# Performance work log

Measured on AMD Instinct MI355X. Metric: run time of the kernel, lower is better.

The kernel has to match this reference:

```python
import jax, jax.numpy as jnp
import numpy as np

PI = 3.14159  # constant used in the torch module
N_QUBITS = 10
N_LAYERS = 4
B = 1024  # number of graphs


def _lin_init(k, fan_in, fan_out):
    k1, k2 = jax.random.split(k)
    s = 1.0 / np.sqrt(fan_in)
    W = jax.random.uniform(k1, (fan_in, fan_out), jnp.float32, -s, s)
    b = jax.random.uniform(k2, (fan_out,), jnp.float32, -s, s)
    return W, b


def setup_inputs():
    key = jax.random.key(0)
    ks = jax.random.split(key, 12)
    N, E, Fin, H, Emb = 32768, 131072, 128, 256, 128
    x = jax.random.normal(ks[0], (N, Fin), jnp.float32)
    edge_index = jax.random.randint(ks[1], (2, E), 0, N)
    batch = jnp.sort(jax.random.randint(ks[2], (N,), 0, B))
    edge_attr = jax.random.uniform(ks[3], (E, 4), dtype=jnp.float32)
    W1, b1 = _lin_init(ks[4], Fin, H)          # GCNConv 1
    W2, b2 = _lin_init(ks[5], H, Emb)          # GCNConv 2
    projW, projb = _lin_init(ks[6], Emb, N_QUBITS)
    vqc_weights = jax.random.uniform(ks[7], (N_LAYERS, N_QUBITS), jnp.float32, 0.0, 2 * np.pi)
    epW, epb = _lin_init(ks[8], 4, N_QUBITS - 1)
    cW1, cb1 = _lin_init(ks[9], Emb + N_QUBITS, 16)
    cW2, cb2 = _lin_init(ks[10], 16, 1)
    return dict(x=x, edge_index=edge_index, batch=batch, edge_attr=edge_attr,
                W1=W1, b1=b1, W2=W2, b2=b2, projW=projW, projb=projb,
                vqc_weights=vqc_weights, epW=epW, epb=epb,
                cW1=cW1, cb1=cb1, cW2=cW2, cb2=cb2)


def _gcn_conv(x, W, b, src, dst, n):
    # GCNConv with self-loops: sym-normalized aggregation of xW
    h = x @ W
    deg = jnp.zeros((n,), x.dtype).at[dst].add(1.0) + 1.0  # +1 self-loop
    dinv = jax.lax.rsqrt(deg)
    coef = (dinv[src] * dinv[dst])[:, None]
    agg = jnp.zeros_like(h).at[dst].add(h[src] * coef)
    return agg + h * (1.0 / deg)[:, None] + b


def _segment_mean(v, seg, n):
    tot = jnp.zeros((n, v.shape[1]), v.dtype).at[seg].add(v)
    cnt = jnp.zeros((n,), v.dtype).at[seg].add(1.0)
    return tot / jnp.clip(cnt, 1.0)[:, None]


def _run_vqc(q_in, weights, ep):
    # Batched real state-vector simulation. All gates (RY, CRY) are real.
    # Wire 0 = most significant bit (pennylane default.qubit convention).
    b = q_in.shape[0]
    dim = 2 ** N_QUBITS
    st = jnp.zeros((b, dim), q_in.dtype).at[:, 0].set(1.0)

    def ry(st, theta, w):
        th = jnp.broadcast_to(theta, (b,)) * 0.5
        c = jnp.cos(th)[:, None, None]
        s = jnp.sin(th)[:, None, None]
        r = st.reshape(b, 2 ** w, 2, -1)
        a0, a1 = r[:, :, 0], r[:, :, 1]
        return jnp.stack([c * a0 - s * a1, s * a0 + c * a1], axis=2).reshape(b, dim)

    def cry(st, theta, w):
        # control w, target w+1 (adjacent wires)
        th = jnp.broadcast_to(theta, (b,)) * 0.5
        c = jnp.cos(th)[:, None, None]
        s = jnp.sin(th)[:, None, None]
        r = st.reshape(b, 2 ** w, 2, 2, -1)
        a0, a1 = r[:, :, 1, 0], r[:, :, 1, 1]
        r = r.at[:, :, 1, 0].set(c * a0 - s * a1).at[:, :, 1, 1].set(s * a0 + c * a1)
        return r.reshape(b, dim)

    for i in range(N_QUBITS):                      # AngleEmbedding (RY)
        st = ry(st, q_in[:, i], i)
    for layer in range(N_LAYERS):
        for i in range(N_QUBITS):
            st = ry(st, weights[layer, i], i)
        for i in range(N_QUBITS - 1):
            st = cry(st, ep[:, i], i)

    probs = st * st
    zs = []
    for i in range(N_QUBITS):
        p = probs.reshape(b, 2 ** i, 2, -1).sum(axis=(1, 3))
        zs.append(p[:, 0] - p[:, 1])               # <PauliZ(i)>
    return jnp.stack(zs, axis=1)                   # [B, n_qubits]


def reference(x, edge_index, batch, edge_attr, W1, b1, W2, b2, projW, projb,
              vqc_weights, epW, epb, cW1, cb1, cW2, cb2):
    N = x.shape[0]
    src, dst = edge_index[0], edge_index[1]
    # GCN encoder: two GCNConv + ReLU, global mean pool (dropout = eval mode)
    h = jax.nn.relu(_gcn_conv(x, W1, b1, src, dst, N))
    h = jax.nn.relu(_gcn_conv(h, W2, b2, src, dst, N))
    emb = _segment_mean(h, batch, B)               # [B, gcn_embed]

    q_in = jnp.tanh(emb @ projW + projb) * PI      # [B, n_qubits]

    # scatter-mean edge pooling per graph, then edge projection
    edge_batch = batch[src]
    pooled_edge = _segment_mean(edge_attr, edge_batch, B)  # [B, 4]
    ep = pooled_edge @ epW + epb                   # [B, n_qubits-1]

    q_out = _run_vqc(q_in, vqc_weights, ep)        # [B, n_qubits]

    combined = jnp.concatenate([emb, q_out], axis=-1)
    hid = jax.nn.relu(combined @ cW1 + cb1)
    return hid @ cW2 + cb2                         # [B, num_tasks]
```

## Files before the change

### kernel.cpp

```cpp
#include <hip/hip_runtime.h>

#define PI_F 3.14159f
#define NQ 10
#define PB 64

__global__ void k_zero(float4* __restrict__ p, int n4) {
  int i = blockIdx.x * blockDim.x + threadIdx.x;
  int stride = gridDim.x * blockDim.x;
  float4 z = {0.f, 0.f, 0.f, 0.f};
  for (; i < n4; i += stride) p[i] = z;
}

__global__ void k_count(const int* __restrict__ dstA, int E, int* __restrict__ cnt) {
  int e = blockIdx.x * blockDim.x + threadIdx.x;
  if (e < E) atomicAdd(&cnt[dstA[e]], 1);
}

__global__ __launch_bounds__(1024) void k_edge_pool(const int* __restrict__ srcA,
                                                    const int* __restrict__ batch,
                                                    const float* __restrict__ eattr, int E,
                                                    float* __restrict__ part) {
  __shared__ float bins[1024 * 5];
  int t = threadIdx.x;
  for (int i = t; i < 5120; i += 1024) bins[i] = 0.f;
  __syncthreads();
  int per = (E + gridDim.x - 1) / gridDim.x;
  int base = blockIdx.x * per;
  int end = min(base + per, E);
  for (int e = base + t; e < end; e += 1024) {
    int s = srcA[e];
    int g = batch[s];
    float4 v = *(const float4*)(eattr + (size_t)e * 4);
    atomicAdd(&bins[g * 5 + 0], v.x);
    atomicAdd(&bins[g * 5 + 1], v.y);
    atomicAdd(&bins[g * 5 + 2], v.z);
    atomicAdd(&bins[g * 5 + 3], v.w);
    atomicAdd(&bins[g * 5 + 4], 1.0f);
  }
  __syncthreads();
  float* dst = part + (size_t)blockIdx.x * 5120;
  for (int i = t; i < 5120; i += 1024) dst[i] = bins[i];
}

__global__ __launch_bounds__(1024) void k_scan1(const int* __restrict__ cnt,
                                                int* __restrict__ incl,
                                                int* __restrict__ bsum) {
  __shared__ int buf[1024];
  int t = threadIdx.x;
  int base = blockIdx.x << 10;
  buf[t] = cnt[base + t];
  __syncthreads();
#pragma unroll
  for (int off = 1; off < 1024; off <<= 1) {
    int x = (t >= off) ? buf[t - off] : 0;
    __syncthreads();
    buf[t] += x;
    __syncthreads();
  }
  incl[base + t] = buf[t];
  if (t == 1023) bsum[blockIdx.x] = buf[t];
}

__global__ void k_node_setup(const int* __restrict__ cnt, const int* __restrict__ incl,
                             const int* __restrict__ bsum, const int* __restrict__ batch,
                             int N, int Bn, int* __restrict__ rowStart,
                             int* __restrict__ pos, float* __restrict__ dinv,
                             float* __restrict__ invdeg, int* __restrict__ starts) {
  int i = blockIdx.x * blockDim.x + threadIdx.x;
  if (i >= N) return;
  int blk = i >> 10;
  int pre = 0;
  for (int j = 0; j < blk; j++) pre += bsum[j];
  int c = cnt[i];
  int inc = incl[i] + pre;
  rowStart[i + 1] = inc;
  pos[i] = inc - c;
  if (i == 0) rowStart[0] = 0;
  float d = (float)c + 1.0f;
  dinv[i] = 1.0f / sqrtf(d);
  invdeg[i] = 1.0f / d;
  int b = batch[i];
  int bp = (i == 0) ? -1 : batch[i - 1];
  for (int g = bp + 1; g <= b; g++) starts[g] = i;
  if (i == N - 1) {
    for (int g = b + 1; g <= Bn; g++) starts[g] = N;
  }
}

__global__ void k_fill(const int* __restrict__ dst, const int* __restrict__ srcA,
                       const float* __restrict__ dinv, int E, int* __restrict__ pos,
                       int* __restrict__ srcSorted, float* __restrict__ dcoef) {
  int e = blockIdx.x * blockDim.x + threadIdx.x;
  if (e >= E) return;
  int s = srcA[e];
  int slot = atomicAdd(&pos[dst[e]], 1);
  srcSorted[slot] = s;
  dcoef[slot] = dinv[s];
}

__global__ __launch_bounds__(256) void k_gemm(const float* __restrict__ A,
                                              const float* __restrict__ B,
                                              float* __restrict__ C,
                                              int M, int K, int N) {
  __shared__ float As[128][33];
  __shared__ float Bs[32][68];
  int t = threadIdx.x;
  int tx = t & 15, ty = t >> 4;
  int row0 = blockIdx.y * 128, col0 = blockIdx.x * 64;
  float acc[8][4] = {};
  for (int k0 = 0; k0 < K; k0 += 32) {
    __syncthreads();
#pragma unroll
    for (int rep = 0; rep < 4; rep++) {
      int slot = t + rep * 256;
      int r = slot >> 3;
      int cg = (slot & 7) << 2;
      float4 v = *(const float4*)(A + (size_t)(row0 + r) * K + (k0 + cg));
      As[r][cg + 0] = v.x;
      As[r][cg + 1] = v.y;
      As[r][cg + 2] = v.z;
      As[r][cg + 3] = v.w;
    }
#pragma unroll
    for (int rep = 0; rep < 2; rep++) {
      int slot = t + rep * 256;
      int r2 = slot >> 4;
      int c2 = (slot & 15) << 2;
      float4 w = *(const float4*)(B + (size_t)(k0 + r2) * N + (col0 + c2));
      *(float4*)&Bs[r2][c2] = w;
    }
    __syncthreads();
#pragma unroll 4
    for (int kk = 0; kk < 32; kk++) {
      float4 b4 = *(const float4*)&Bs[kk][tx << 2];
      float bv[4] = {b4.x, b4.y, b4.z, b4.w};
      float av[8];
#pragma unroll
      for (int i = 0; i < 8; i++) av[i] = As[(ty << 3) + i][kk];
#pragma unroll
      for (int i = 0; i < 8; i++)
#pragma unroll
        for (int j = 0; j < 4; j++) acc[i][j] = fmaf(av[i], bv[j], acc[i][j]);
    }
  }
#pragma unroll
  for (int i = 0; i < 8; i++) {
    float4 v = {acc[i][0], acc[i][1], acc[i][2], acc[i][3]};
    *(float4*)(C + (size_t)(row0 + (ty << 3) + i) * N + (col0 + (tx << 2))) = v;
  }
}

__global__ __launch_bounds__(256) void k_gcn_combine(
    const float* __restrict__ hlin, const int* __restrict__ srcSorted,
    const float* __restrict__ dcoef, const int* __restrict__ rowStart,
    const float* __restrict__ dinv, const float* __restrict__ invdeg,
    const float* __restrict__ bias, float* __restrict__ hout, int N, int C, int shift) {
  int gid = blockIdx.x * blockDim.x + threadIdx.x;
  int n = gid >> shift;
  if (n >= N) return;
  int cq = (gid & ((1 << shift) - 1)) << 2;
  int e0 = rowStart[n], e1 = rowStart[n + 1];
  float di = dinv[n];
  float ax = 0.f, ay = 0.f, az = 0.f, aw = 0.f;
  for (int e = e0; e < e1; e++) {
    int s = srcSorted[e];
    float coef = dcoef[e] * di;
    float4 v = *(const float4*)(hlin + (size_t)s * C + cq);
    ax = fmaf(coef, v.x, ax);
    ay = fmaf(coef, v.y, ay);
    az = fmaf(coef, v.z, az);
    aw = fmaf(coef, v.w, aw);
  }
  float idg = invdeg[n];
  float4 hv = *(const float4*)(hlin + (size_t)n * C + cq);
  float4 bv = *(const float4*)(bias + cq);
  float4 r;
  r.x = fmaxf(fmaf(hv.x, idg, ax) + bv.x, 0.f);
  r.y = fmaxf(fmaf(hv.y, idg, ay) + bv.y, 0.f);
  r.z = fmaxf(fmaf(hv.z, idg, az) + bv.z, 0.f);
  r.w = fmaxf(fmaf(hv.w, idg, aw) + bv.w, 0.f);
  *(float4*)(hout + (size_t)n * C + cq) = r;
}

__global__ __launch_bounds__(256) void k_segmean(const float* __restrict__ h2,
                                                 const int* __restrict__ starts,
                                                 float* __restrict__ emb) {
  __shared__ float tmp[128];
  int g = blockIdx.x;
  int t = threadIdx.x;
  int c = t & 127;
  int half = t >> 7;
  int s0 = starts[g], s1 = starts[g + 1];
  float inv = 1.0f / (float)(s1 - s0 > 0 ? s1 - s0 : 1);
  float sum = 0.f;
  for (int i = s0 + half; i < s1; i += 2) sum += h2[(size_t)i * 128 + c];
  if (half == 0) tmp[c] = sum;
  __syncthreads();
  if (half == 1) emb[(size_t)g * 128 + c] = (tmp[c] + sum) * inv;
}

__global__ __launch_bounds__(256) void k_angles(
    const float* __restrict__ emb, const float* __restrict__ part,
    const float* __restrict__ projW, const float* __restrict__ projb,
    const float* __restrict__ epW, const float* __restrict__ epb, int Bn,
    float* __restrict__ angc, float* __restrict__ angs) {
  int wid = (blockIdx.x * blockDim.x + threadIdx.x) >> 6;
  int lane = threadIdx.x & 63;
  int g = wid / 11;
  int a = wid - g * 11;
  if (g >= Bn) return;
  if (a < 10) {
    float2 v = *(const float2*)(emb + (size_t)g * 128 + lane * 2);
    float s = v.x * projW[(lane * 2) * NQ + a] + v.y * projW[(lane * 2 + 1) * NQ + a];
#pragma unroll
    for (int off = 32; off >= 1; off >>= 1) s += __shfl_down(s, off, 64);
    if (lane == 0) {
      float th = tanhf(s + projb[a]) * PI_F * 0.5f;
      angc[g * 19 + a] = cosf(th);
      angs[g * 19 + a] = sinf(th);
    }
  } else {
    const float* pp = part + (size_t)lane * 5120 + g * 5;
    float p0 = pp[0], p1 = pp[1], p2 = pp[2], p3 = pp[3], p4 = pp[4];
#pragma unroll
    for (int off = 32; off >= 1; off >>= 1) {
      p0 += __shfl_down(p0, off, 64);
      p1 += __shfl_down(p1, off, 64);
      p2 += __shfl_down(p2, off, 64);
      p3 += __shfl_down(p3, off, 64);
      p4 += __shfl_down(p4, off, 64);
    }
    p0 = __shfl(p0, 0, 64);
    p1 = __shfl(p1, 0, 64);
    p2 = __shfl(p2, 0, 64);
    p3 = __shfl(p3, 0, 64);
    p4 = __shfl(p4, 0, 64);
    if (lane < 9) {
      float icnt = 1.0f / fmaxf(p4, 1.0f);
      float sum = epb[lane];
      sum = fmaf(p0 * icnt, epW[0 * 9 + lane], sum);
      sum = fmaf(p1 * icnt, epW[1 * 9 + lane], sum);
      sum = fmaf(p2 * icnt, epW[2 * 9 + lane], sum);
      sum = fmaf(p3 * icnt, epW[3 * 9 + lane], sum);
      float th = sum * 0.5f;
      angc[g * 19 + 10 + lane] = cosf(th);
      angs[g * 19 + 10 + lane] = sinf(th);
    }
  }
}

template <int B>
__device__ __forceinline__ void ry_reg(float* st, float c, float s) {
#pragma unroll
  for (int j = 0; j < 16; j++) {
    if (!(j & (1 << B))) {
      float x0 = st[j], x1 = st[j | (1 << B)];
      st[j] = c * x0 - s * x1;
      st[j | (1 << B)] = fmaf(s, x0, c * x1);
    }
  }
}

template <int LB>
__device__ __forceinline__ void ry_lane(float* st, float c, float s, int lane) {
  bool hi = (lane >> LB) & 1;
#pragma unroll
  for (int j = 0; j < 16; j++) {
    float p = __shfl_xor(st[j], 1 << LB, 64);
    float a = c * st[j] - s * p;
    float b = fmaf(s, p, c * st[j]);
    st[j] = hi ? b : a;
  }
}

template <int LC, int LT>
__device__ __forceinline__ void cry_ll(float* st, float c, float s, int lane) {
  bool ctrl = (lane >> LC) & 1;
  bool hi = (lane >> LT) & 1;
#pragma unroll
  for (int j = 0; j < 16; j++) {
    float p = __shfl_xor(st[j], 1 << LT, 64);
    float a = c * st[j] - s * p;
    float b = fmaf(s, p, c * st[j]);
    float nv = hi ? b : a;
    st[j] = ctrl ? nv : st[j];
  }
}

__device__ __forceinline__ void cry_l0r3(float* st, float c, float s, int lane) {
  bool ctrl = lane & 1;
#pragma unroll
  for (int j = 0; j < 8; j++) {
    float x0 = st[j], x1 = st[j + 8];
    float n0 = c * x0 - s * x1;
    float n1 = fmaf(s, x0, c * x1);
    st[j] = ctrl ? n0 : x0;
    st[j + 8] = ctrl ? n1 : x1;
  }
}

template <int BC, int BT>
__device__ __forceinline__ void cry_rr(float* st, float c, float s) {
#pragma unroll
  for (int j = 0; j < 16; j++) {
    if ((j & (1 << BC)) && !(j & (1 << BT))) {
      float x0 = st[j], x1 = st[j | (1 << BT)];
      st[j] = c * x0 - s * x1;
      st[j | (1 << BT)] = fmaf(s, x0, c * x1);
    }
  }
}

__global__ __launch_bounds__(64) void k_vqc_head(
    const float* __restrict__ emb, const float* __restrict__ angc,
    const float* __restrict__ angs, const float* __restrict__ vqcW,
    const float* __restrict__ cW1, const float* __restrict__ cb1,
    const float* __restrict__ cW2, const float* __restrict__ cb2,
    float* __restrict__ out) {
  int g = blockIdx.x;
  int lane = threadIdx.x;
  __shared__ float semb[128];
  __shared__ float csc[59], css[59];
  __shared__ float zq[NQ];

  {
    float2 v = *(const float2*)(emb + (size_t)g * 128 + lane * 2);
    semb[lane * 2] = v.x;
    semb[lane * 2 + 1] = v.y;
  }
  if (lane < NQ) {
    csc[lane] = angc[g * 19 + lane];
    css[lane] = angs[g * 19 + lane];
  } else if (lane < 50) {
    float th = vqcW[lane - NQ] * 0.5f;
    csc[lane] = cosf(th);
    css[lane] = sinf(th);
  } else if (lane < 59) {
    csc[lane] = angc[g * 19 + 10 + (lane - 50)];
    css[lane] = angs[g * 19 + 10 + (lane - 50)];
  }
  __syncthreads();

  float st[16];
#pragma unroll
  for (int j = 0; j < 16; j++) st[j] = 0.f;
  if (lane == 0) st[0] = 1.f;

#pragma unroll 1
  for (int L = 0; L < 5; L++) {
    int b = L * 10;
    ry_lane<5>(st, csc[b + 0], css[b + 0], lane);
    ry_lane<4>(st, csc[b + 1], css[b + 1], lane);
    ry_lane<3>(st, csc[b + 2], css[b + 2], lane);
    ry_lane<2>(st, csc[b + 3], css[b + 3], lane);
    ry_lane<1>(st, csc[b + 4], css[b + 4], lane);
    ry_lane<0>(st, csc[b + 5], css[b + 5], lane);
    ry_reg<3>(st, csc[b + 6], css[b + 6]);
    ry_reg<2>(st, csc[b + 7], css[b + 7]);
    ry_reg<1>(st, csc[b + 8], css[b + 8]);
    ry_reg<0>(st, csc[b + 9], css[b + 9]);
    if (b) {
      cry_ll<5, 4>(st, csc[50], css[50], lane);
      cry_ll<4, 3>(st, csc[51], css[51], lane);
      cry_ll<3, 2>(st, csc[52], css[52], lane);
      cry_ll<2, 1>(st, csc[53], css[53], lane);
      cry_ll<1, 0>(st, csc[54], css[54], lane);
      cry_l0r3(st, csc[55], css[55], lane);
      cry_rr<3, 2>(st, csc[56], css[56]);
      cry_rr<2, 1>(st, csc[57], css[57]);
      cry_rr<1, 0>(st, csc[58], css[58]);
    }
  }

  float p[16];
  float tot = 0.f;
#pragma unroll
  for (int j = 0; j < 16; j++) {
    p[j] = st[j] * st[j];
    tot += p[j];
  }
  float z[NQ];
#pragma unroll
  for (int i = 0; i < 6; i++) {
    int LB = 5 - i;
    z[i] = ((lane >> LB) & 1) ? -tot : tot;
  }
#pragma unroll
  for (int i = 6; i < 10; i++) {
    int B = 9 - i;
    float a = 0.f;
#pragma unroll
    for (int j = 0; j < 16; j++) a += ((j >> B) & 1) ? -p[j] : p[j];
    z[i] = a;
  }
#pragma unroll
  for (int off = 32; off >= 1; off >>= 1)
#pragma unroll
    for (int i = 0; i < 10; i++) z[i] += __shfl_down(z[i], off, 64);
  if (lane == 0) {
#pragma unroll
    for (int i = 0; i < 10; i++) zq[i] = z[i];
  }
  __syncthreads();

  int o = lane & 15, cch = lane >> 4;
  float sum = 0.f;
#pragma unroll
  for (int t = 0; t < 32; t++) {
    int k = cch * 32 + t;
    sum = fmaf(semb[k], cW1[k * 16 + o], sum);
  }
  if (cch == 3) {
#pragma unroll
    for (int k = 0; k < 10; k++) sum = fmaf(zq[k], cW1[(128 + k) * 16 + o], sum);
  }
  sum += __shfl_down(sum, 32, 64);
  sum += __shfl_down(sum, 16, 64);
  float hv = fmaxf(sum + cb1[o], 0.f);
  float ov = (lane < 16) ? hv * cW2[lane] : 0.f;
  ov += __shfl_down(ov, 8, 64);
  ov += __shfl_down(ov, 4, 64);
  ov += __shfl_down(ov, 2, 64);
  ov += __shfl_down(ov, 1, 64);
  if (lane == 0) out[g] = ov + cb2[0];
}

extern "C" void kernel_launch(void* const* d_in, const int* in_sizes, int n_in,
                              void* d_out, int out_size, void* d_ws, size_t ws_size,
                              hipStream_t stream) {
  const float* x = (const float*)d_in[0];
  const int* ei = (const int*)d_in[1];
  const int* batch = (const int*)d_in[2];
  const float* eattr = (const float*)d_in[3];
  const float* W1 = (const float*)d_in[4];
  const float* b1 = (const float*)d_in[5];
  const float* W2 = (const float*)d_in[6];
  const float* b2 = (const float*)d_in[7];
  const float* projW = (const float*)d_in[8];
  const float* projb = (const float*)d_in[9];
  const float* vqcW = (const float*)d_in[10];
  const float* epW = (const float*)d_in[11];
  const float* epb = (const float*)d_in[12];
  const float* cW1 = (const float*)d_in[13];
  const float* cb1 = (const float*)d_in[14];
  const float* cW2 = (const float*)d_in[15];
  const float* cb2 = (const float*)d_in[16];
  float* out = (float*)d_out;

  const int N = in_sizes[0] / 128;
  const int E = in_sizes[1] / 2;
  const int Bn = out_size;

  const int* srcA = ei;
  const int* dstA = ei + E;

  char* ws = (char*)d_ws;
  float* bufA = (float*)ws;
  float* bufB = (float*)(ws + ((size_t)32 << 20));
  size_t off = (size_t)64 << 20;
  auto alloc = [&](size_t bytes) {
    size_t o = off;
    off += (bytes + 255) & ~(size_t)255;
    return o;
  };
  int* cnt = (int*)(ws + alloc((size_t)N * 4));
  size_t zeroEnd = off;
  float* part = (float*)(ws + alloc((size_t)PB * 5120 * 4));
  int* rowStart = (int*)(ws + alloc((size_t)(N + 1) * 4));
  int* pos = (int*)(ws + alloc((size_t)N * 4));
  int* srcSorted = (int*)(ws + alloc((size_t)E * 4));
  float* dcoef = (float*)(ws + alloc((size_t)E * 4));
  float* dinv = (float*)(ws + alloc((size_t)N * 4));
  float* invdeg = (float*)(ws + alloc((size_t)N * 4));
  int* starts = (int*)(ws + alloc((size_t)(Bn + 1) * 4));
  int* incl = (int*)(ws + alloc((size_t)N * 4));
  int* bsum = (int*)(ws + alloc(64 * 4));
  float* emb = (float*)(ws + alloc((size_t)Bn * 128 * 4));
  float* angc = (float*)(ws + alloc((size_t)Bn * 19 * 4));
  float* angs = (float*)(ws + alloc((size_t)Bn * 19 * 4));

  int eblocks = (E + 255) / 256;
  int nblocks = (N + 255) / 256;
  int nb1024 = N >> 10;

  int zero4 = (int)((zeroEnd - ((size_t)64 << 20)) / 16);
  k_zero<<<(zero4 + 255) / 256, 256, 0, stream>>>((float4*)(ws + ((size_t)64 << 20)), zero4);

  k_count<<<eblocks, 256, 0, stream>>>(dstA, E, cnt);
  k_edge_pool<<<PB, 1024, 0, stream>>>(srcA, batch, eattr, E, part);
  k_scan1<<<nb1024, 1024, 0, stream>>>(cnt, incl, bsum);
  k_node_setup<<<nblocks, 256, 0, stream>>>(cnt, incl, bsum, batch, N, Bn, rowStart, pos,
                                            dinv, invdeg, starts);
  k_fill<<<eblocks, 256, 0, stream>>>(dstA, srcA, dinv, E, pos, srcSorted, dcoef);

  {
    dim3 grid(256 / 64, N / 128);
    k_gemm<<<grid, 256, 0, stream>>>(x, W1, bufA, N, 128, 256);
  }
  k_gcn_combine<<<(N * 64) / 256, 256, 0, stream>>>(bufA, srcSorted, dcoef, rowStart,
                                                    dinv, invdeg, b1, bufB, N, 256, 6);
  {
    dim3 grid(128 / 64, N / 128);
    k_gemm<<<grid, 256, 0, stream>>>(bufB, W2, bufA, N, 256, 128);
  }
  k_gcn_combine<<<(N * 32) / 256, 256, 0, stream>>>(bufA, srcSorted, dcoef, rowStart,
                                                    dinv, invdeg, b2, bufB, N, 128, 5);
  k_segmean<<<Bn, 256, 0, stream>>>(bufB, starts, emb);
  {
    int waves = Bn * 11;
    k_angles<<<(waves + 3) / 4, 256, 0, stream>>>(emb, part, projW, projb, epW, epb, Bn,
                                                  angc, angs);
  }
  k_vqc_head<<<Bn, 64, 0, stream>>>(emb, angc, angs, vqcW, cW1, cb1, cW2, cb2, out);
}
```

Measured before the change: 207.8 us.

## Replace FP32 SIMT GEMMs with split-bf16 MFMA GEMMs using hi/lo decomposition

Both dense GEMMs move from scalar FP32 FMA tiles to MFMA bf16 instructions. Each operand is split into a bf16 high part and a bf16 residual, and three MFMAs per tile pair (hi*hi, hi*lo, lo*hi) recover near-FP32 accuracy. The first GCN combine kernel now writes the hi/lo bf16 pair directly, so the second GEMM needs no separate split pass. This trades extra split kernels for x and the weights, and more bf16 buffers, for much higher matrix throughput.

```diff
diff --git a/kernel.cpp b/kernel.cpp
--- a/kernel.cpp
+++ b/kernel.cpp
@@ -1,14 +1,40 @@
 #include <hip/hip_runtime.h>
+#include <hip/hip_bf16.h>
 
 #define PI_F 3.14159f
 #define NQ 10
 #define PB 64
+
+typedef __attribute__((ext_vector_type(8))) short short8v;
+typedef __attribute__((ext_vector_type(4))) float f32x4;
 
 __global__ void k_zero(float4* __restrict__ p, int n4) {
   int i = blockIdx.x * blockDim.x + threadIdx.x;
   int stride = gridDim.x * blockDim.x;
   float4 z = {0.f, 0.f, 0.f, 0.f};
   for (; i < n4; i += stride) p[i] = z;
+}
+
+__global__ void k_split(const float4* __restrict__ src, ushort4* __restrict__ hi,
+                        ushort4* __restrict__ lo, int n4) {
+  int i = blockIdx.x * blockDim.x + threadIdx.x;
+  int stride = gridDim.x * blockDim.x;
+  for (; i < n4; i += stride) {
+    float4 v = src[i];
+    ushort4 h, l;
+    float f, r;
+    __hip_bfloat16 b;
+    f = v.x; b = __float2bfloat16(f); h.x = *(ushort*)&b;
+    r = f - __bfloat162float(b); b = __float2bfloat16(r); l.x = *(ushort*)&b;
+    f = v.y; b = __float2bfloat16(f); h.y = *(ushort*)&b;
+    r = f - __bfloat162float(b); b = __float2bfloat16(r); l.y = *(ushort*)&b;
+    f = v.z; b = __float2bfloat16(f); h.z = *(ushort*)&b;
+    r = f - __bfloat162float(b); b = __float2bfloat16(r); l.z = *(ushort*)&b;
+    f = v.w; b = __float2bfloat16(f); h.w = *(ushort*)&b;
+    r = f - __bfloat162float(b); b = __float2bfloat16(r); l.w = *(ushort*)&b;
+    hi[i] = h;
+    lo[i] = l;
+  }
 }
 
 __global__ void k_count(const int* __restrict__ dstA, int E, int* __restrict__ cnt) {
@@ -98,63 +124,91 @@
   dcoef[slot] = dinv[s];
 }
 
-__global__ __launch_bounds__(256) void k_gemm(const float* __restrict__ A,
-                                              const float* __restrict__ B,
-                                              float* __restrict__ C,
-                                              int M, int K, int N) {
-  __shared__ float As[128][33];
-  __shared__ float Bs[32][68];
+template <int K>
+__global__ __launch_bounds__(256) void k_gemm_mfma(
+    const ushort* __restrict__ Ahi, const ushort* __restrict__ Alo,
+    const ushort* __restrict__ Bhi, const ushort* __restrict__ Blo,
+    float* __restrict__ C, int M, int N) {
+  __shared__ ushort Ah[128][40], Al[128][40];
+  __shared__ ushort Bh[128][40], Bl[128][40];
   int t = threadIdx.x;
-  int tx = t & 15, ty = t >> 4;
-  int row0 = blockIdx.y * 128, col0 = blockIdx.x * 64;
-  float acc[8][4] = {};
+  int wid = t >> 6, lane = t & 63;
+  int wr = wid >> 1, wc = wid & 1;
+  int row0 = blockIdx.y * 128, col0 = blockIdx.x * 128;
+
+  f32x4 acc[4][4];
+#pragma unroll
+  for (int i = 0; i < 4; i++)
+#pragma unroll
+    for (int j = 0; j < 4; j++) acc[i][j] = (f32x4){0.f, 0.f, 0.f, 0.f};
+
   for (int k0 = 0; k0 < K; k0 += 32) {
     __syncthreads();
 #pragma unroll
-    for (int rep = 0; rep < 4; rep++) {
-      int slot = t + rep * 256;
-      int r = slot >> 3;
-      int cg = (slot & 7) << 2;
-      float4 v = *(const float4*)(A + (size_t)(row0 + r) * K + (k0 + cg));
-      As[r][cg + 0] = v.x;
-      As[r][cg + 1] = v.y;
-      As[r][cg + 2] = v.z;
-      As[r][cg + 3] = v.w;
-    }
-#pragma unroll
     for (int rep = 0; rep < 2; rep++) {
-      int slot = t + rep * 256;
-      int r2 = slot >> 4;
-      int c2 = (slot & 15) << 2;
-      float4 w = *(const float4*)(B + (size_t)(k0 + r2) * N + (col0 + c2));
-      *(float4*)&Bs[r2][c2] = w;
+      int s = t + rep * 256;
+      int r = s >> 2;
+      int kg = (s & 3) << 3;
+      *(uint4*)&Ah[r][kg] = *(const uint4*)(Ahi + (size_t)(row0 + r) * K + k0 + kg);
+      *(uint4*)&Al[r][kg] = *(const uint4*)(Alo + (size_t)(row0 + r) * K + k0 + kg);
+    }
+#pragma unroll
+    for (int rep = 0; rep < 2; rep++) {
+      int s = t + rep * 256;
+      int kr = s >> 4;
+      int cg = (s & 15) << 3;
+      uint4 wh = *(const uint4*)(Bhi + (size_t)(k0 + kr) * N + col0 + cg);
+      uint4 wl = *(const uint4*)(Blo + (size_t)(k0 + kr) * N + col0 + cg);
+      const ushort* ph = (const ushort*)&wh;
+      const ushort* pl = (const ushort*)&wl;
+#pragma unroll
+      for (int i = 0; i < 8; i++) {
+        Bh[cg + i][kr] = ph[i];
+        Bl[cg + i][kr] = pl[i];
+      }
     }
     __syncthreads();
-#pragma unroll 4
-    for (int kk = 0; kk < 32; kk++) {
-      float4 b4 = *(const float4*)&Bs[kk][tx << 2];
-      float bv[4] = {b4.x, b4.y, b4.z, b4.w};
-      float av[8];
-#pragma unroll
-      for (int i = 0; i < 8; i++) av[i] = As[(ty << 3) + i][kk];
-#pragma unroll
-      for (int i = 0; i < 8; i++)
-#pragma unroll
-        for (int j = 0; j < 4; j++) acc[i][j] = fmaf(av[i], bv[j], acc[i][j]);
-    }
-  }
-#pragma unroll
-  for (int i = 0; i < 8; i++) {
-    float4 v = {acc[i][0], acc[i][1], acc[i][2], acc[i][3]};
-    *(float4*)(C + (size_t)(row0 + (ty << 3) + i) * N + (col0 + (tx << 2))) = v;
-  }
+
+    int kgrp = (lane >> 4) << 3;
+    short8v afh[4], afl[4], bfh[4], bfl[4];
+#pragma unroll
+    for (int f = 0; f < 4; f++) {
+      int ar = wr * 64 + f * 16 + (lane & 15);
+      afh[f] = *(const short8v*)&Ah[ar][kgrp];
+      afl[f] = *(const short8v*)&Al[ar][kgrp];
+      int bc = wc * 64 + f * 16 + (lane & 15);
+      bfh[f] = *(const short8v*)&Bh[bc][kgrp];
+      bfl[f] = *(const short8v*)&Bl[bc][kgrp];
+    }
+#pragma unroll
+    for (int fr = 0; fr < 4; fr++)
+#pragma unroll
+      for (int fc = 0; fc < 4; fc++) {
+        acc[fr][fc] = __builtin_amdgcn_mfma_f32_16x16x32_bf16(afh[fr], bfh[fc], acc[fr][fc], 0, 0, 0);
+        acc[fr][fc] = __builtin_amdgcn_mfma_f32_16x16x32_bf16(afh[fr], bfl[fc], acc[fr][fc], 0, 0, 0);
+        acc[fr][fc] = __builtin_amdgcn_mfma_f32_16x16x32_bf16(afl[fr], bfh[fc], acc[fr][fc], 0, 0, 0);
+      }
+  }
+
+#pragma unroll
+  for (int fr = 0; fr < 4; fr++)
+#pragma unroll
+    for (int fc = 0; fc < 4; fc++) {
+      int col = col0 + wc * 64 + fc * 16 + (lane & 15);
+#pragma unroll
+      for (int j = 0; j < 4; j++) {
+        int row = row0 + wr * 64 + fr * 16 + ((lane >> 4) << 2) + j;
+        C[(size_t)row * N + col] = acc[fr][fc][j];
+      }
+    }
 }
 
 __global__ __launch_bounds__(256) void k_gcn_combine(
     const float* __restrict__ hlin, const int* __restrict__ srcSorted,
     const float* __restrict__ dcoef, const int* __restrict__ rowStart,
     const float* __restrict__ dinv, const float* __restrict__ invdeg,
-    const float* __restrict__ bias, float* __restrict__ hout, int N, int C, int shift) {
+    const float* __restrict__ bias, float* __restrict__ hout,
+    ushort* __restrict__ houtHi, ushort* __restrict__ houtLo, int N, int C, int shift) {
   int gid = blockIdx.x * blockDim.x + threadIdx.x;
   int n = gid >> shift;
   if (n >= N) return;
@@ -179,7 +233,23 @@
   r.y = fmaxf(fmaf(hv.y, idg, ay) + bv.y, 0.f);
   r.z = fmaxf(fmaf(hv.z, idg, az) + bv.z, 0.f);
   r.w = fmaxf(fmaf(hv.w, idg, aw) + bv.w, 0.f);
-  *(float4*)(hout + (size_t)n * C + cq) = r;
+  if (houtHi) {
+    ushort4 h, l;
+    float f, rr;
+    __hip_bfloat16 b;
+    f = r.x; b = __float2bfloat16(f); h.x = *(ushort*)&b;
+    rr = f - __bfloat162float(b); b = __float2bfloat16(rr); l.x = *(ushort*)&b;
+    f = r.y; b = __float2bfloat16(f); h.y = *(ushort*)&b;
+    rr = f - __bfloat162float(b); b = __float2bfloat16(rr); l.y = *(ushort*)&b;
+    f = r.z; b = __float2bfloat16(f); h.z = *(ushort*)&b;
+    rr = f - __bfloat162float(b); b = __float2bfloat16(rr); l.z = *(ushort*)&b;
+    f = r.w; b = __float2bfloat16(f); h.w = *(ushort*)&b;
+    rr = f - __bfloat162float(b); b = __float2bfloat16(rr); l.w = *(ushort*)&b;
+    *(ushort4*)(houtHi + (size_t)n * C + cq) = h;
+    *(ushort4*)(houtLo + (size_t)n * C + cq) = l;
+  } else {
+    *(float4*)(hout + (size_t)n * C + cq) = r;
+  }
 }
 
 __global__ __launch_bounds__(256) void k_segmean(const float* __restrict__ h2,
@@ -478,6 +548,14 @@
   float* emb = (float*)(ws + alloc((size_t)Bn * 128 * 4));
   float* angc = (float*)(ws + alloc((size_t)Bn * 19 * 4));
   float* angs = (float*)(ws + alloc((size_t)Bn * 19 * 4));
+  ushort* xhi = (ushort*)(ws + alloc((size_t)N * 128 * 2));
+  ushort* xlo = (ushort*)(ws + alloc((size_t)N * 128 * 2));
+  ushort* h1hi = (ushort*)(ws + alloc((size_t)N * 256 * 2));
+  ushort* h1lo = (ushort*)(ws + alloc((size_t)N * 256 * 2));
+  ushort* w1hi = (ushort*)(ws + alloc((size_t)128 * 256 * 2));
+  ushort* w1lo = (ushort*)(ws + alloc((size_t)128 * 256 * 2));
+  ushort* w2hi = (ushort*)(ws + alloc((size_t)256 * 128 * 2));
+  ushort* w2lo = (ushort*)(ws + alloc((size_t)256 * 128 * 2));
 
   int eblocks = (E + 255) / 256;
   int nblocks = (N + 255) / 256;
@@ -493,18 +571,27 @@
                                             dinv, invdeg, starts);
   k_fill<<<eblocks, 256, 0, stream>>>(dstA, srcA, dinv, E, pos, srcSorted, dcoef);
 
+  k_split<<<2048, 256, 0, stream>>>((const float4*)x, (ushort4*)xhi, (ushort4*)xlo,
+                                    N * 128 / 4);
+  k_split<<<32, 256, 0, stream>>>((const float4*)W1, (ushort4*)w1hi, (ushort4*)w1lo,
+                                  128 * 256 / 4);
+  k_split<<<32, 256, 0, stream>>>((const float4*)W2, (ushort4*)w2hi, (ushort4*)w2lo,
+                                  256 * 128 / 4);
+
   {
-    dim3 grid(256 / 64, N / 128);
-    k_gemm<<<grid, 256, 0, stream>>>(x, W1, bufA, N, 128, 256);
+    dim3 grid(256 / 128, N / 128);
+    k_gemm_mfma<128><<<grid, 256, 0, stream>>>(xhi, xlo, w1hi, w1lo, bufA, N, 256);
   }
   k_gcn_combine<<<(N * 64) / 256, 256, 0, stream>>>(bufA, srcSorted, dcoef, rowStart,
-                                                    dinv, invdeg, b1, bufB, N, 256, 6);
+                                                    dinv, invdeg, b1, nullptr, h1hi, h1lo,
+                                                    N, 256, 6);
   {
-    dim3 grid(128 / 64, N / 128);
-    k_gemm<<<grid, 256, 0, stream>>>(bufB, W2, bufA, N, 256, 128);
+    dim3 grid(128 / 128, N / 128);
+    k_gemm_mfma<256><<<grid, 256, 0, stream>>>(h1hi, h1lo, w2hi, w2lo, bufA, N, 128);
   }
   k_gcn_combine<<<(N * 32) / 256, 256, 0, stream>>>(bufA, srcSorted, dcoef, rowStart,
-                                                    dinv, invdeg, b2, bufB, N, 128, 5);
+                                                    dinv, invdeg, b2, bufB, nullptr,
+                                                    nullptr, N, 128, 5);
   k_segmean<<<Bn, 256, 0, stream>>>(bufB, starts, emb);
   {
     int waves = Bn * 11;
```

Result: faster. 202.8 us (-2.4%).
